# Kernel optimization log

Hardware: AMD Instinct MI355X
Metric: run time of the kernel (lower is better)

Reference implementation:

```python
import jax, jax.numpy as jnp
import numpy as np

D_MODEL = 1024
NUM_HEADS = 16
D_K = D_MODEL // NUM_HEADS
D_FF = 4096
EPS = 1e-5


def setup_inputs() -> dict:
    key = jax.random.key(0)
    ks = jax.random.split(key, 16)
    B, S = 2, 2048
    s_attn = 1.0 / np.sqrt(D_MODEL)
    s_ff1 = 1.0 / np.sqrt(D_MODEL)
    s_ff2 = 1.0 / np.sqrt(D_FF)
    return {
        "x": jax.random.normal(ks[0], (B, S, D_MODEL), jnp.float32),
        "Wq": jax.random.normal(ks[1], (D_MODEL, D_MODEL), jnp.float32) * s_attn,
        "bq": jnp.zeros((D_MODEL,), jnp.float32),
        "Wk": jax.random.normal(ks[2], (D_MODEL, D_MODEL), jnp.float32) * s_attn,
        "bk": jnp.zeros((D_MODEL,), jnp.float32),
        "Wv": jax.random.normal(ks[3], (D_MODEL, D_MODEL), jnp.float32) * s_attn,
        "bv": jnp.zeros((D_MODEL,), jnp.float32),
        "Wo": jax.random.normal(ks[4], (D_MODEL, D_MODEL), jnp.float32) * s_attn,
        "bo": jnp.zeros((D_MODEL,), jnp.float32),
        "W1": jax.random.normal(ks[5], (D_MODEL, D_FF), jnp.float32) * s_ff1,
        "b1": jnp.zeros((D_FF,), jnp.float32),
        "W2": jax.random.normal(ks[6], (D_FF, D_MODEL), jnp.float32) * s_ff2,
        "b2": jnp.zeros((D_MODEL,), jnp.float32),
        "g1": jnp.ones((D_MODEL,), jnp.float32),
        "be1": jnp.zeros((D_MODEL,), jnp.float32),
        "g2": jnp.ones((D_MODEL,), jnp.float32),
        "be2": jnp.zeros((D_MODEL,), jnp.float32),
    }


def _layernorm(x, g, b):
    m = jnp.mean(x, axis=-1, keepdims=True)
    v = jnp.mean(jnp.square(x - m), axis=-1, keepdims=True)
    return (x - m) * jax.lax.rsqrt(v + EPS) * g + b


def _split_heads(x, B, S):
    # (B, S, D) -> (B, H, S, d_k)
    return x.reshape(B, S, NUM_HEADS, D_K).transpose(0, 2, 1, 3)


def reference(x, Wq, bq, Wk, bk, Wv, bv, Wo, bo, W1, b1, W2, b2, g1, be1, g2, be2):
    B, S, _ = x.shape
    Q = _split_heads(x @ Wq + bq, B, S)
    K = _split_heads(x @ Wk + bk, B, S)
    V = _split_heads(x @ Wv + bv, B, S)
    scores = jnp.einsum("bhqd,bhkd->bhqk", Q, K) / np.sqrt(D_K).astype(np.float32)
    attn = jax.nn.softmax(scores, axis=-1)  # dropout is identity (p=0 / eval)
    ctx = jnp.einsum("bhqk,bhkd->bhqd", attn, V)
    ctx = ctx.transpose(0, 2, 1, 3).reshape(B, S, D_MODEL)
    attn_out = ctx @ Wo + bo
    h = _layernorm(x + attn_out, g1, be1)
    ff = jax.nn.relu(h @ W1 + b1) @ W2 + b2
    out = _layernorm(h + ff, g2, be2)
    return out, attn
```

## Files before the change

### kernel.cpp

```cpp
#include <hip/hip_runtime.h>
#include <cstddef>
#include <cstdint>

#define D_MODEL 1024
#define NUM_HEADS 16
#define DK 64
#define D_FF 4096
#define SEQ 2048
#define BATCH 2
#define EPS 1e-5f

typedef unsigned short u16;
typedef __attribute__((ext_vector_type(8))) short bf16x8;
typedef __attribute__((ext_vector_type(8))) unsigned short us8;
typedef __attribute__((ext_vector_type(4))) unsigned short us4;
typedef __attribute__((ext_vector_type(4))) float f32x4;

#define SBAR() asm volatile("s_barrier" ::: "memory")

__device__ __forceinline__ u16 f2b(float f) {
    unsigned u = __float_as_uint(f);
    u += 0x7fffu + ((u >> 16) & 1u);
    return (u16)(u >> 16);
}
__device__ __forceinline__ float b2f(u16 v) {
    return __uint_as_float((unsigned)v << 16);
}

__device__ __forceinline__ void gload16(const void* g, void* l) {
    __builtin_amdgcn_global_load_lds(
        (const __attribute__((address_space(1))) void*)g,
        (__attribute__((address_space(3))) void*)l, 16, 0, 0);
}

__device__ __forceinline__ void stage_half(
    const u16* __restrict__ g, int ld, long kbase, int h,
    u16* dst, int tid, int wid)
{
#pragma unroll
    for (int r = 0; r < 2; ++r) {
        const int ci  = r * 512 + tid;
        const int row = ci >> 2;
        const int wd  = ci & 3;
        const int f   = (row + (row >> 2)) & 3;
        const long src = (long)row * ld + kbase + (long)(h * 4 + (wd ^ f)) * 8;
        gload16(g + src, dst + (r * 512 + wid * 64) * 8);
    }
}

__device__ __forceinline__ bf16x8 frag64(const u16* base, int ks, int row, int g) {
    const int f = (row + (row >> 2)) & 3;
    return *(const bf16x8*)&base[ks * 8192 + row * 32 + ((g ^ f) * 8)];
}

template<int KTOT, bool RELU, int NSPLIT>
__global__ __launch_bounds__(512, 2) void gemm256(
    const u16* __restrict__ Abf, const u16* __restrict__ BT,
    const float* __restrict__ bias0, const float* __restrict__ bias1,
    const float* __restrict__ bias2,
    u16* __restrict__ C0, u16* __restrict__ C1, u16* __restrict__ C2,
    int ldc, int nx)
{
    constexpr int NT = KTOT / 64;
    __shared__ u16 lds[2][32768];

    const int tid = threadIdx.x;
    const int wid = tid >> 6, l = tid & 63;
    const int r16 = l & 15, g = l >> 4;
    const int wr = wid >> 2, wc = wid & 3;

    const int nwg = gridDim.x;
    const int q = nwg >> 3, rr = nwg & 7;
    const int xcd = blockIdx.x & 7, idx = blockIdx.x >> 3;
    const int wg = (xcd < rr ? xcd * (q + 1) : rr * (q + 1) + (xcd - rr) * q) + idx;
    const long bm = (long)(wg / nx) * 256;
    const long bn = (long)(wg % nx) * 256;

    const u16* Ag = Abf + bm * KTOT;
    const u16* Bg = BT + bn * KTOT;

    f32x4 acc[8][4];
#pragma unroll
    for (int i = 0; i < 8; ++i)
#pragma unroll
        for (int n = 0; n < 4; ++n)
            acc[i][n] = (f32x4){0.f, 0.f, 0.f, 0.f};

    stage_half(Ag, KTOT, 0, 0, &lds[0][0],     tid, wid);
    stage_half(Ag, KTOT, 0, 1, &lds[0][8192],  tid, wid);
    stage_half(Bg, KTOT, 0, 0, &lds[0][16384], tid, wid);
    stage_half(Bg, KTOT, 0, 1, &lds[0][24576], tid, wid);
    if (NT > 1) {
        stage_half(Ag, KTOT, 64, 0, &lds[1][0],     tid, wid);
        stage_half(Bg, KTOT, 64, 0, &lds[1][16384], tid, wid);
    }
    asm volatile("s_waitcnt vmcnt(4)" ::: "memory");
    SBAR();

    for (int t = 0; t < NT; ++t) {
        u16* cur = &lds[t & 1][0];
        u16* nxt = &lds[(t + 1) & 1][0];
        const long k1 = (long)(t + 1) * 64;
        const long k2 = (long)(t + 2) * 64;
        const bool s1 = (t + 1 < NT), s2 = (t + 2 < NT);

        bf16x8 a0[4], b0[4];
#pragma unroll
        for (int i = 0; i < 4; ++i) {
            a0[i] = frag64(cur,         0, wr * 128 + i * 16 + r16, g);
            b0[i] = frag64(cur + 16384, 0, wc * 64  + i * 16 + r16, g);
        }
        if (s1) stage_half(Ag, KTOT, k1, 1, nxt + 8192, tid, wid);
        SBAR();
        __builtin_amdgcn_s_setprio(1);
#pragma unroll
        for (int i = 0; i < 4; ++i)
#pragma unroll
            for (int n = 0; n < 4; ++n)
                acc[i][n] = __builtin_amdgcn_mfma_f32_16x16x32_bf16(
                    a0[i], b0[n], acc[i][n], 0, 0, 0);
        __builtin_amdgcn_s_setprio(0);
        SBAR();

        bf16x8 a1[4];
#pragma unroll
        for (int i = 0; i < 4; ++i)
            a1[i] = frag64(cur, 0, wr * 128 + (i + 4) * 16 + r16, g);
        if (s1) stage_half(Bg, KTOT, k1, 1, nxt + 24576, tid, wid);
        SBAR();
        __builtin_amdgcn_s_setprio(1);
#pragma unroll
        for (int i = 0; i < 4; ++i)
#pragma unroll
            for (int n = 0; n < 4; ++n)
                acc[i + 4][n] = __builtin_amdgcn_mfma_f32_16x16x32_bf16(
                    a1[i], b0[n], acc[i + 4][n], 0, 0, 0);
        __builtin_amdgcn_s_setprio(0);
        SBAR();

        bf16x8 a2[4], b1[4];
#pragma unroll
        for (int i = 0; i < 4; ++i) {
            a2[i] = frag64(cur,         1, wr * 128 + i * 16 + r16, g);
            b1[i] = frag64(cur + 16384, 1, wc * 64  + i * 16 + r16, g);
        }
        if (s2) stage_half(Ag, KTOT, k2, 0, cur, tid, wid);
        SBAR();
        __builtin_amdgcn_s_setprio(1);
#pragma unroll
        for (int i = 0; i < 4; ++i)
#pragma unroll
            for (int n = 0; n < 4; ++n)
                acc[i][n] = __builtin_amdgcn_mfma_f32_16x16x32_bf16(
                    a2[i], b1[n], acc[i][n], 0, 0, 0);
        __builtin_amdgcn_s_setprio(0);
        SBAR();

        bf16x8 a3[4];
#pragma unroll
        for (int i = 0; i < 4; ++i)
            a3[i] = frag64(cur, 1, wr * 128 + (i + 4) * 16 + r16, g);
        if (s2) stage_half(Bg, KTOT, k2, 0, cur + 16384, tid, wid);
        SBAR();
        __builtin_amdgcn_s_setprio(1);
#pragma unroll
        for (int i = 0; i < 4; ++i)
#pragma unroll
            for (int n = 0; n < 4; ++n)
                acc[i + 4][n] = __builtin_amdgcn_mfma_f32_16x16x32_bf16(
                    a3[i], b1[n], acc[i + 4][n], 0, 0, 0);
        __builtin_amdgcn_s_setprio(0);
        if (s2)      asm volatile("s_waitcnt vmcnt(4)" ::: "memory");
        else if (s1) asm volatile("s_waitcnt vmcnt(0)" ::: "memory");
        SBAR();
    }

    u16* Cb = C0; const float* bp = bias0; long coff = 0;
    if (NSPLIT == 3) {
        const int grp = (int)(bn >> 10);
        if (grp == 1)      { Cb = C1; bp = bias1; }
        else if (grp == 2) { Cb = C2; bp = bias2; }
        coff = (long)grp << 10;
    }
    const long crow0 = bm + wr * 128 + g * 4;
    const long ccol0 = bn + wc * 64 + r16 - coff;
#pragma unroll
    for (int n = 0; n < 4; ++n) {
        const long col = ccol0 + n * 16;
        const float bv = bp[col];
#pragma unroll
        for (int i = 0; i < 8; ++i)
#pragma unroll
            for (int j = 0; j < 4; ++j) {
                const long row = crow0 + i * 16 + j;
                float v = acc[i][n][j] + bv;
                if (RELU) v = fmaxf(v, 0.f);
                Cb[row * (long)ldc + col] = f2b(v);
            }
    }
}

template<int BM, int BN, int OM, bool RELU>
__global__ __launch_bounds__(256) void gemm_mfma(
    const u16* __restrict__ Abf, const u16* __restrict__ BT,
    const float* __restrict__ bias, void* __restrict__ Cout,
    int lda, int ldb, int ldc, int K, int nx)
{
    constexpr int WN = (BN >= 128) ? 2 : 1;
    constexpr int WM = 4 / WN;
    constexpr int MI = BM / (WM * 16);
    constexpr int NI = BN / (WN * 16);
    constexpr int RA = (BM * 4) / 256;
    constexpr int RB = (BN * 4) / 256;
    constexpr int TILE = (BM + BN) * 32;

    __shared__ u16 sm[2][TILE];

    const int tid = threadIdx.x;
    const int w = tid >> 6, l = tid & 63;
    const int r16 = l & 15, g = l >> 4;
    const int wr = w / WN, wc = w % WN;

    const int nwg = gridDim.x;
    const int q = nwg >> 3, rr = nwg & 7;
    const int xcd = blockIdx.x & 7, idx = blockIdx.x >> 3;
    const int wg = (xcd < rr ? xcd * (q + 1) : rr * (q + 1) + (xcd - rr) * q) + idx;
    const long bm = (long)(wg / nx) * BM;
    const long bn = (long)(wg % nx) * BN;

    f32x4 acc[MI][NI];
#pragma unroll
    for (int mi = 0; mi < MI; ++mi)
#pragma unroll
        for (int ni = 0; ni < NI; ++ni)
            acc[mi][ni] = (f32x4){0.f, 0.f, 0.f, 0.f};

    long aOff[RA], bOff[RB];
#pragma unroll
    for (int r = 0; r < RA; ++r) {
        int c = r * 256 + tid;
        aOff[r] = (long)(bm + (c >> 2)) * lda + (c & 3) * 8;
    }
#pragma unroll
    for (int r = 0; r < RB; ++r) {
        int c = r * 256 + tid;
        bOff[r] = (long)(bn + (c >> 2)) * ldb + (c & 3) * 8;
    }

#pragma unroll
    for (int r = 0; r < RA; ++r)
        gload16(Abf + aOff[r], &sm[0][0] + (r * 256 + w * 64) * 8);
#pragma unroll
    for (int r = 0; r < RB; ++r)
        gload16(BT + bOff[r], &sm[0][BM * 32] + (r * 256 + w * 64) * 8);
    __syncthreads();

    int cur = 0;
    for (int k0 = 0; k0 < K; k0 += 32) {
        if (k0 + 32 < K) {
            const int nxt = cur ^ 1;
#pragma unroll
            for (int r = 0; r < RA; ++r)
                gload16(Abf + aOff[r] + k0 + 32, &sm[nxt][0] + (r * 256 + w * 64) * 8);
#pragma unroll
            for (int r = 0; r < RB; ++r)
                gload16(BT + bOff[r] + k0 + 32, &sm[nxt][BM * 32] + (r * 256 + w * 64) * 8);
        }

        const u16* smA = &sm[cur][0];
        const u16* smB = &sm[cur][BM * 32];
        bf16x8 af[MI], bfr[NI];
#pragma unroll
        for (int mi = 0; mi < MI; ++mi)
            af[mi] = *(const bf16x8*)&smA[(wr * (MI * 16) + mi * 16 + r16) * 32 + g * 8];
#pragma unroll
        for (int ni = 0; ni < NI; ++ni)
            bfr[ni] = *(const bf16x8*)&smB[(wc * (NI * 16) + ni * 16 + r16) * 32 + g * 8];
#pragma unroll
        for (int mi = 0; mi < MI; ++mi)
#pragma unroll
            for (int ni = 0; ni < NI; ++ni)
                acc[mi][ni] = __builtin_amdgcn_mfma_f32_16x16x32_bf16(
                    af[mi], bfr[ni], acc[mi][ni], 0, 0, 0);

        __syncthreads();
        cur ^= 1;
    }

    float* Cf = (float*)Cout;
    u16*   Cb = (u16*)Cout;
    const long crow0 = bm + wr * (MI * 16) + g * 4;
    const long ccol0 = bn + wc * (NI * 16) + r16;
#pragma unroll
    for (int ni = 0; ni < NI; ++ni) {
        const long col = ccol0 + ni * 16;
        const float bv = bias ? bias[col] : 0.f;
#pragma unroll
        for (int mi = 0; mi < MI; ++mi) {
#pragma unroll
            for (int j = 0; j < 4; ++j) {
                const long row = crow0 + mi * 16 + j;
                float v = acc[mi][ni][j] + bv;
                if (RELU) v = fmaxf(v, 0.f);
                if (OM == 0) Cf[row * (long)ldc + col] = v;
                else         Cb[row * (long)ldc + col] = f2b(v);
            }
        }
    }
}

#define QBLK 128
#define KBLK 64
#define NTT (SEQ / KBLK)
#define C2E 0.18033688f

__global__ __launch_bounds__(256) void flash_attn(
    const u16* __restrict__ Qg, const u16* __restrict__ Kg,
    const u16* __restrict__ Vt, float* __restrict__ attn,
    u16* __restrict__ ctx)
{
    __shared__ u16 smem[16384];
    __shared__ u16 Ps[4][2048];
    __shared__ float stats[4][32];

    u16* const Qs  = smem;
    u16* const kb0 = smem + 8192;
    u16* const kb1 = smem;

    const int tid = threadIdx.x;
    const int w = tid >> 6, l = tid & 63;
    const int r16 = l & 15, g = l >> 4;

    const int wg = (blockIdx.x & 7) * (gridDim.x >> 3) + (blockIdx.x >> 3);
    const int qb = wg & 15, z = wg >> 4;
    const int b = z >> 4, h = z & 15;
    const long q0 = (long)qb * QBLK;

    const long kBase = ((long)b * SEQ) * D_MODEL + h * DK;
    const long vBase = (long)z * DK * SEQ;

#pragma unroll
    for (int r = 0; r < 4; ++r) {
        int c = r * 256 + tid;
        int row = c >> 3, bl = c & 7;
        long src = ((long)b * SEQ + q0 + row) * D_MODEL + h * DK
                 + ((bl ^ (row & 7)) * 8);
        gload16(Qg + src, Qs + (r * 256 + w * 64) * 8);
    }
#pragma unroll
    for (int r = 0; r < 2; ++r) {
        int c = r * 256 + tid;
        int row = c >> 3, bl = c & 7;
        gload16(Kg + kBase + (long)row * D_MODEL + ((bl ^ (row & 7)) * 8),
                kb0 + (r * 256 + w * 64) * 8);
    }
    __syncthreads();

    bf16x8 qf[2][2];
#pragma unroll
    for (int qi = 0; qi < 2; ++qi)
#pragma unroll
        for (int ks = 0; ks < 2; ++ks)
            qf[qi][ks] = *(const bf16x8*)
                &Qs[(w * 32 + qi * 16 + r16) * 64 + (((ks * 4 + g) ^ (r16 & 7)) * 8)];
    __syncthreads();

    float lrun[2] = {0.f, 0.f};

    for (int t = 0; t < NTT; ++t) {
        if (t + 1 < NTT) {
            u16* kdst = ((t + 1) & 1) ? kb1 : kb0;
            const long kro = (long)(t + 1) * KBLK;
#pragma unroll
            for (int r = 0; r < 2; ++r) {
                int c = r * 256 + tid;
                int row = c >> 3, bl = c & 7;
                gload16(Kg + kBase + (kro + row) * D_MODEL + ((bl ^ (row & 7)) * 8),
                        kdst + (r * 256 + w * 64) * 8);
            }
        }
        const u16* kcur = (t & 1) ? kb1 : kb0;

        f32x4 sT[4][2];
#pragma unroll
        for (int ki = 0; ki < 4; ++ki)
#pragma unroll
            for (int qi = 0; qi < 2; ++qi) sT[ki][qi] = (f32x4){0.f, 0.f, 0.f, 0.f};

        __builtin_amdgcn_s_setprio(1);
#pragma unroll
        for (int ks = 0; ks < 2; ++ks) {
            bf16x8 kf[4];
#pragma unroll
            for (int ki = 0; ki < 4; ++ki)
                kf[ki] = *(const bf16x8*)
                    &kcur[(ki * 16 + r16) * 64 + (((ks * 4 + g) ^ (r16 & 7)) * 8)];
#pragma unroll
            for (int ki = 0; ki < 4; ++ki)
#pragma unroll
                for (int qi = 0; qi < 2; ++qi)
                    sT[ki][qi] = __builtin_amdgcn_mfma_f32_16x16x32_bf16(
                        kf[ki], qf[qi][ks], sT[ki][qi], 0, 0, 0);
        }
        __builtin_amdgcn_s_setprio(0);

#pragma unroll
        for (int qi = 0; qi < 2; ++qi) {
            float ls = 0.f;
#pragma unroll
            for (int ki = 0; ki < 4; ++ki)
#pragma unroll
                for (int j = 0; j < 4; ++j)
                    ls += exp2f(sT[ki][qi][j] * C2E);
            ls += __shfl_xor(ls, 16);
            ls += __shfl_xor(ls, 32);
            lrun[qi] += ls;
        }
        __syncthreads();
    }

    u16* const p2b0 = smem + 8192;
    u16* const p2b1 = smem;
#pragma unroll
    for (int r = 0; r < 2; ++r) {
        int c = r * 256 + tid;
        int row = c >> 3, bl = c & 7;
        gload16(Kg + kBase + (long)row * D_MODEL + ((bl ^ (row & 7)) * 8),
                p2b0 + (r * 256 + w * 64) * 8);
        gload16(Vt + vBase + (long)row * SEQ + ((bl ^ (row & 7)) * 8),
                p2b0 + 4096 + (r * 256 + w * 64) * 8);
    }
    if (l < 16) {
        stats[w][r16]      = 1.0f / lrun[0];
        stats[w][16 + r16] = 1.0f / lrun[1];
    }
    __syncthreads();

    float il2[2][4];
#pragma unroll
    for (int mi = 0; mi < 2; ++mi)
#pragma unroll
        for (int j = 0; j < 4; ++j)
            il2[mi][j] = stats[w][mi * 16 + g * 4 + j];

    f32x4 acc2[2][4];
#pragma unroll
    for (int mi = 0; mi < 2; ++mi)
#pragma unroll
        for (int ni = 0; ni < 4; ++ni) acc2[mi][ni] = (f32x4){0.f, 0.f, 0.f, 0.f};

    for (int t = 0; t < NTT; ++t) {
        const int k0 = t * KBLK;
        if (t + 1 < NTT) {
            u16* dst = ((t + 1) & 1) ? p2b1 : p2b0;
            const long kro = (long)(t + 1) * KBLK;
#pragma unroll
            for (int r = 0; r < 2; ++r) {
                int c = r * 256 + tid;
                int row = c >> 3, bl = c & 7;
                gload16(Kg + kBase + (kro + row) * D_MODEL + ((bl ^ (row & 7)) * 8),
                        dst + (r * 256 + w * 64) * 8);
                gload16(Vt + vBase + (long)row * SEQ + kro + ((bl ^ (row & 7)) * 8),
                        dst + 4096 + (r * 256 + w * 64) * 8);
            }
        }
        const u16* kcur = (t & 1) ? p2b1 : p2b0;
        const u16* vcur = kcur + 4096;

        f32x4 s[2][4];
#pragma unroll
        for (int mi = 0; mi < 2; ++mi)
#pragma unroll
            for (int ni = 0; ni < 4; ++ni) s[mi][ni] = (f32x4){0.f, 0.f, 0.f, 0.f};

        __builtin_amdgcn_s_setprio(1);
#pragma unroll
        for (int ks = 0; ks < 2; ++ks) {
            bf16x8 kf[4];
#pragma unroll
            for (int ni = 0; ni < 4; ++ni)
                kf[ni] = *(const bf16x8*)
                    &kcur[(ni * 16 + r16) * 64 + (((ks * 4 + g) ^ (r16 & 7)) * 8)];
#pragma unroll
            for (int mi = 0; mi < 2; ++mi)
#pragma unroll
                for (int ni = 0; ni < 4; ++ni)
                    s[mi][ni] = __builtin_amdgcn_mfma_f32_16x16x32_bf16(
                        qf[mi][ks], kf[ni], s[mi][ni], 0, 0, 0);
        }
        __builtin_amdgcn_s_setprio(0);

#pragma unroll
        for (int mi = 0; mi < 2; ++mi)
#pragma unroll
            for (int j = 0; j < 4; ++j) {
                const int pr = mi * 16 + g * 4 + j;
                const long grow = (long)z * SEQ + q0 + w * 32 + pr;
#pragma unroll
                for (int ni = 0; ni < 4; ++ni) {
                    float p = exp2f(s[mi][ni][j] * C2E) * il2[mi][j];
                    const int pc = ni * 16 + r16;
                    attn[grow * SEQ + k0 + pc] = p;
                    Ps[w][pr * 64 + (pc ^ ((pr & 7) << 3))] = f2b(p);
                }
            }

        __builtin_amdgcn_s_setprio(1);
#pragma unroll
        for (int ks = 0; ks < 2; ++ks) {
            bf16x8 pf[2], vf[4];
#pragma unroll
            for (int mi = 0; mi < 2; ++mi)
                pf[mi] = *(const bf16x8*)
                    &Ps[w][(mi * 16 + r16) * 64 + (((ks * 4 + g) ^ (r16 & 7)) * 8)];
#pragma unroll
            for (int ni = 0; ni < 4; ++ni)
                vf[ni] = *(const bf16x8*)
                    &vcur[(ni * 16 + r16) * 64 + (((ks * 4 + g) ^ (r16 & 7)) * 8)];
#pragma unroll
            for (int mi = 0; mi < 2; ++mi)
#pragma unroll
                for (int ni = 0; ni < 4; ++ni)
                    acc2[mi][ni] = __builtin_amdgcn_mfma_f32_16x16x32_bf16(
                        pf[mi], vf[ni], acc2[mi][ni], 0, 0, 0);
        }
        __builtin_amdgcn_s_setprio(0);
        __syncthreads();
    }

#pragma unroll
    for (int mi = 0; mi < 2; ++mi)
#pragma unroll
        for (int j = 0; j < 4; ++j) {
            const long grow = (long)b * SEQ + q0 + w * 32 + mi * 16 + g * 4 + j;
#pragma unroll
            for (int ni = 0; ni < 4; ++ni)
                ctx[grow * D_MODEL + h * DK + ni * 16 + r16] = f2b(acc2[mi][ni][j]);
        }
}

__global__ __launch_bounds__(256) void cvt_bf16_kernel(
    const float* __restrict__ in, u16* __restrict__ out, long n)
{
    long i = ((long)blockIdx.x * 256 + threadIdx.x) * 8;
    if (i >= n) return;
    float4 a = *(const float4*)(in + i);
    float4 b = *(const float4*)(in + i + 4);
    us8 o;
    o[0] = f2b(a.x); o[1] = f2b(a.y); o[2] = f2b(a.z); o[3] = f2b(a.w);
    o[4] = f2b(b.x); o[5] = f2b(b.y); o[6] = f2b(b.z); o[7] = f2b(b.w);
    *(us8*)(out + i) = o;
}

__global__ __launch_bounds__(256) void transpose_cvt(
    const float* __restrict__ W, u16* __restrict__ Wt, int R, int C)
{
    __shared__ float t[32][33];
    const int tx = threadIdx.x & 31, ty = threadIdx.x >> 5;
    const long c = (long)blockIdx.x * 32 + tx;
    const long r0 = (long)blockIdx.y * 32;
#pragma unroll
    for (int j = 0; j < 32; j += 8)
        t[ty + j][tx] = W[(r0 + ty + j) * C + c];
    __syncthreads();
    const long r = r0 + tx;
#pragma unroll
    for (int j = 0; j < 32; j += 8)
        Wt[((long)blockIdx.x * 32 + ty + j) * R + r] = f2b(t[tx][ty + j]);
}

__global__ __launch_bounds__(256) void transpose_cvt4(
    const float* __restrict__ W0, const float* __restrict__ W1,
    const float* __restrict__ W2, const float* __restrict__ W3,
    u16* __restrict__ dst)
{
    __shared__ float t[32][33];
    const int z = blockIdx.z;
    const float* W = (z == 0) ? W0 : (z == 1) ? W1 : (z == 2) ? W2 : W3;
    u16* Wt = dst + (size_t)z * D_MODEL * D_MODEL;
    const int tx = threadIdx.x & 31, ty = threadIdx.x >> 5;
    const long c = (long)blockIdx.x * 32 + tx;
    const long r0 = (long)blockIdx.y * 32;
#pragma unroll
    for (int j = 0; j < 32; j += 8)
        t[ty + j][tx] = W[(r0 + ty + j) * D_MODEL + c];
    __syncthreads();
    const long r = r0 + tx;
#pragma unroll
    for (int j = 0; j < 32; j += 8)
        Wt[((long)blockIdx.x * 32 + ty + j) * D_MODEL + r] = f2b(t[tx][ty + j]);
}

__global__ __launch_bounds__(256) void transpose_v(
    const u16* __restrict__ V, u16* __restrict__ Vt)
{
    __shared__ u16 t[32][33];
    const int z = blockIdx.z, b = z >> 4, h = z & 15;
    const int tx = threadIdx.x & 31, ty = threadIdx.x >> 5;
    const long k0 = (long)blockIdx.x * 32;
    const long d0 = (long)blockIdx.y * 32;
#pragma unroll
    for (int j = 0; j < 32; j += 8)
        t[ty + j][tx] = V[((long)b * SEQ + k0 + ty + j) * D_MODEL + h * DK + d0 + tx];
    __syncthreads();
#pragma unroll
    for (int j = 0; j < 32; j += 8)
        Vt[((long)z * DK + d0 + ty + j) * SEQ + k0 + tx] = t[tx][ty + j];
}

template<bool BBF, bool WB>
__global__ __launch_bounds__(256) void add_ln_kernel(
    const float* __restrict__ a, const void* __restrict__ bsrc,
    const float* __restrict__ g, const float* __restrict__ be,
    float* __restrict__ out32, u16* __restrict__ outbf)
{
    const int l = threadIdx.x & 63, w = threadIdx.x >> 6;
    const long row = (long)blockIdx.x * 4 + w;
    const long base = row * D_MODEL;

    float xv[16];
#pragma unroll
    for (int c = 0; c < 4; ++c) {
        const long off = c * 256 + l * 4;
        float4 av = *(const float4*)(a + base + off);
        float4 bv;
        if (BBF) {
            us4 bb = *(const us4*)((const u16*)bsrc + base + off);
            bv.x = b2f(bb[0]); bv.y = b2f(bb[1]);
            bv.z = b2f(bb[2]); bv.w = b2f(bb[3]);
        } else {
            bv = *(const float4*)((const float*)bsrc + base + off);
        }
        xv[c * 4 + 0] = av.x + bv.x; xv[c * 4 + 1] = av.y + bv.y;
        xv[c * 4 + 2] = av.z + bv.z; xv[c * 4 + 3] = av.w + bv.w;
    }

    float s = 0.f;
#pragma unroll
    for (int i = 0; i < 16; ++i) s += xv[i];
#pragma unroll
    for (int off = 1; off < 64; off <<= 1) s += __shfl_xor(s, off);
    const float mean = s * (1.0f / D_MODEL);

    float ss = 0.f;
#pragma unroll
    for (int i = 0; i < 16; ++i) {
        xv[i] -= mean;
        ss += xv[i] * xv[i];
    }
#pragma unroll
    for (int off = 1; off < 64; off <<= 1) ss += __shfl_xor(ss, off);
    const float rs = rsqrtf(ss * (1.0f / D_MODEL) + EPS);

#pragma unroll
    for (int c = 0; c < 4; ++c) {
        const long off = c * 256 + l * 4;
        float4 gv = *(const float4*)(g + off);
        float4 bev = *(const float4*)(be + off);
        float4 o;
        o.x = xv[c * 4 + 0] * rs * gv.x + bev.x;
        o.y = xv[c * 4 + 1] * rs * gv.y + bev.y;
        o.z = xv[c * 4 + 2] * rs * gv.z + bev.z;
        o.w = xv[c * 4 + 3] * rs * gv.w + bev.w;
        *(float4*)&out32[base + off] = o;
        if (WB) {
            us4 ob;
            ob[0] = f2b(o.x); ob[1] = f2b(o.y);
            ob[2] = f2b(o.z); ob[3] = f2b(o.w);
            *(us4*)&outbf[base + off] = ob;
        }
    }
}

extern "C" void kernel_launch(void* const* d_in, const int* in_sizes, int n_in,
                              void* d_out, int out_size, void* d_ws, size_t ws_size,
                              hipStream_t stream)
{
    const float* x   = (const float*)d_in[0];
    const float* Wq  = (const float*)d_in[1];
    const float* bq  = (const float*)d_in[2];
    const float* Wk  = (const float*)d_in[3];
    const float* bk  = (const float*)d_in[4];
    const float* Wv  = (const float*)d_in[5];
    const float* bv  = (const float*)d_in[6];
    const float* Wo  = (const float*)d_in[7];
    const float* bo  = (const float*)d_in[8];
    const float* W1  = (const float*)d_in[9];
    const float* b1  = (const float*)d_in[10];
    const float* W2  = (const float*)d_in[11];
    const float* b2  = (const float*)d_in[12];
    const float* g1  = (const float*)d_in[13];
    const float* be1 = (const float*)d_in[14];
    const float* g2  = (const float*)d_in[15];
    const float* be2 = (const float*)d_in[16];

    float* out  = (float*)d_out;
    float* attn = out + (size_t)BATCH * SEQ * D_MODEL;

    char* ws = (char*)d_ws;
    const size_t MB = 1u << 20;
    u16* x_bf   = (u16*)(ws);
    u16* Q_bf   = (u16*)(ws + 8 * MB);
    u16* K_bf   = (u16*)(ws + 16 * MB);
    u16* V_bf   = (u16*)(ws + 24 * MB);
    u16* Vt     = (u16*)(ws + 32 * MB);
    u16* Wqt    = (u16*)(ws + 40 * MB);
    u16* Wot    = (u16*)(ws + 46 * MB);
    u16* W1t    = (u16*)(ws + 48 * MB);
    u16* W2t    = (u16*)(ws + 56 * MB);
    u16* ff1_bf = (u16*)(ws + 64 * MB);
    float* h32  = (float*)(ws + 112 * MB);
    u16* ctx_bf = x_bf;
    u16* h_bf   = K_bf;
    u16* ao_bf  = V_bf;
    u16* ff2_bf = Vt;

    const int M = BATCH * SEQ;
    const long MD = (long)M * D_MODEL;
    dim3 T(256);

    cvt_bf16_kernel<<<dim3(MD / 2048), T, 0, stream>>>(x, x_bf, MD);
    transpose_cvt4<<<dim3(32, 32, 4), T, 0, stream>>>(Wq, Wk, Wv, Wo, Wqt);
    transpose_cvt<<<dim3(D_FF / 32, D_MODEL / 32), T, 0, stream>>>(W1, W1t, D_MODEL, D_FF);
    transpose_cvt<<<dim3(D_MODEL / 32, D_FF / 32), T, 0, stream>>>(W2, W2t, D_FF, D_MODEL);

    gemm256<D_MODEL, false, 3><<<dim3((M / 256) * (3 * D_MODEL / 256)), dim3(512), 0, stream>>>(
        x_bf, Wqt, bq, bk, bv, Q_bf, K_bf, V_bf, D_MODEL, 3 * D_MODEL / 256);

    transpose_v<<<dim3(SEQ/32, DK/32, BATCH*NUM_HEADS), T, 0, stream>>>(V_bf, Vt);

    flash_attn<<<dim3((SEQ/QBLK) * BATCH * NUM_HEADS), T, 0, stream>>>(
        Q_bf, K_bf, Vt, attn, ctx_bf);

    gemm_mfma<128,128,1,false><<<dim3((D_MODEL/128) * (M/128)), T, 0, stream>>>(
        ctx_bf, Wot, bo, ao_bf, D_MODEL, D_MODEL, D_MODEL, D_MODEL, D_MODEL/128);

    add_ln_kernel<true,true><<<dim3(M/4), T, 0, stream>>>(x, ao_bf, g1, be1, h32, h_bf);

    gemm256<D_MODEL, true, 1><<<dim3((M / 256) * (D_FF / 256)), dim3(512), 0, stream>>>(
        h_bf, W1t, b1, nullptr, nullptr, ff1_bf, nullptr, nullptr, D_FF, D_FF / 256);

    gemm_mfma<128,128,1,false><<<dim3((D_MODEL/128) * (M/128)), T, 0, stream>>>(
        ff1_bf, W2t, b2, ff2_bf, D_FF, D_FF, D_MODEL, D_FF, D_MODEL/128);

    add_ln_kernel<true,false><<<dim3(M/4), T, 0, stream>>>(h32, ff2_bf, g2, be2, out, nullptr);
}
```

Measured before the change: 440.1 us.

## Merge preprocessing kernels, move QKV to 128-tile GEMM, use bf16 residuals in layernorm

Folds the x conversion and all four weight transposes into one preproc launch. The QKV projection moves from the 256x256 gemm256 kernel to the 128x128 gemm_mfma kernel with a three-way output split, which gives more workgroups. Both add+layernorm kernels now read bf16 residual inputs (x_bf, h_bf) instead of fp32 copies, removing the fp32 h buffer and its traffic at some cost in precision. The attention-probability output is written with nontemporal stores to limit cache pollution from the large attn tensor.

```diff
diff --git a/kernel.cpp b/kernel.cpp
--- a/kernel.cpp
+++ b/kernel.cpp
@@ -53,12 +53,10 @@
     return *(const bf16x8*)&base[ks * 8192 + row * 32 + ((g ^ f) * 8)];
 }
 
-template<int KTOT, bool RELU, int NSPLIT>
+template<int KTOT, bool RELU>
 __global__ __launch_bounds__(512, 2) void gemm256(
     const u16* __restrict__ Abf, const u16* __restrict__ BT,
-    const float* __restrict__ bias0, const float* __restrict__ bias1,
-    const float* __restrict__ bias2,
-    u16* __restrict__ C0, u16* __restrict__ C1, u16* __restrict__ C2,
+    const float* __restrict__ bias0, u16* __restrict__ C0,
     int ldc, int nx)
 {
     constexpr int NT = KTOT / 64;
@@ -175,6 +173,110 @@
         SBAR();
     }
 
+    const long crow0 = bm + wr * 128 + g * 4;
+    const long ccol0 = bn + wc * 64 + r16;
+#pragma unroll
+    for (int n = 0; n < 4; ++n) {
+        const long col = ccol0 + n * 16;
+        const float bv = bias0[col];
+#pragma unroll
+        for (int i = 0; i < 8; ++i)
+#pragma unroll
+            for (int j = 0; j < 4; ++j) {
+                const long row = crow0 + i * 16 + j;
+                float v = acc[i][n][j] + bv;
+                if (RELU) v = fmaxf(v, 0.f);
+                C0[row * (long)ldc + col] = f2b(v);
+            }
+    }
+}
+
+template<bool RELU, int NSPLIT>
+__global__ __launch_bounds__(256) void gemm_mfma(
+    const u16* __restrict__ Abf, const u16* __restrict__ BT,
+    const float* __restrict__ bias0, const float* __restrict__ bias1,
+    const float* __restrict__ bias2,
+    u16* __restrict__ C0, u16* __restrict__ C1, u16* __restrict__ C2,
+    int lda, int ldb, int ldc, int K, int nx)
+{
+    constexpr int BM = 128, BN = 128;
+    constexpr int MI = 4, NI = 4;
+    constexpr int RA = 2, RB = 2;
+    constexpr int TILE = (BM + BN) * 32;
+
+    __shared__ u16 sm[2][TILE];
+
+    const int tid = threadIdx.x;
+    const int w = tid >> 6, l = tid & 63;
+    const int r16 = l & 15, g = l >> 4;
+    const int wr = w >> 1, wc = w & 1;
+
+    const int nwg = gridDim.x;
+    const int q = nwg >> 3, rr = nwg & 7;
+    const int xcd = blockIdx.x & 7, idx = blockIdx.x >> 3;
+    const int wg = (xcd < rr ? xcd * (q + 1) : rr * (q + 1) + (xcd - rr) * q) + idx;
+    const long bm = (long)(wg / nx) * BM;
+    const long bn = (long)(wg % nx) * BN;
+
+    f32x4 acc[MI][NI];
+#pragma unroll
+    for (int mi = 0; mi < MI; ++mi)
+#pragma unroll
+        for (int ni = 0; ni < NI; ++ni)
+            acc[mi][ni] = (f32x4){0.f, 0.f, 0.f, 0.f};
+
+    long aOff[RA], bOff[RB];
+#pragma unroll
+    for (int r = 0; r < RA; ++r) {
+        int c = r * 256 + tid;
+        aOff[r] = (long)(bm + (c >> 2)) * lda + (c & 3) * 8;
+    }
+#pragma unroll
+    for (int r = 0; r < RB; ++r) {
+        int c = r * 256 + tid;
+        bOff[r] = (long)(bn + (c >> 2)) * ldb + (c & 3) * 8;
+    }
+
+#pragma unroll
+    for (int r = 0; r < RA; ++r)
+        gload16(Abf + aOff[r], &sm[0][0] + (r * 256 + w * 64) * 8);
+#pragma unroll
+    for (int r = 0; r < RB; ++r)
+        gload16(BT + bOff[r], &sm[0][BM * 32] + (r * 256 + w * 64) * 8);
+    __syncthreads();
+
+    int cur = 0;
+    for (int k0 = 0; k0 < K; k0 += 32) {
+        if (k0 + 32 < K) {
+            const int nxt = cur ^ 1;
+#pragma unroll
+            for (int r = 0; r < RA; ++r)
+                gload16(Abf + aOff[r] + k0 + 32, &sm[nxt][0] + (r * 256 + w * 64) * 8);
+#pragma unroll
+            for (int r = 0; r < RB; ++r)
+                gload16(BT + bOff[r] + k0 + 32, &sm[nxt][BM * 32] + (r * 256 + w * 64) * 8);
+        }
+
+        const u16* smA = &sm[cur][0];
+        const u16* smB = &sm[cur][BM * 32];
+        bf16x8 af[MI], bfr[NI];
+#pragma unroll
+        for (int mi = 0; mi < MI; ++mi)
+            af[mi] = *(const bf16x8*)&smA[(wr * 64 + mi * 16 + r16) * 32 + g * 8];
+#pragma unroll
+        for (int ni = 0; ni < NI; ++ni)
+            bfr[ni] = *(const bf16x8*)&smB[(wc * 64 + ni * 16 + r16) * 32 + g * 8];
+#pragma unroll
+        for (int mi = 0; mi < MI; ++mi)
+#pragma unroll
+            for (int ni = 0; ni < NI; ++ni)
+                acc[mi][ni] = __builtin_amdgcn_mfma_f32_16x16x32_bf16(
+                    af[mi], bfr[ni], acc[mi][ni], 0, 0, 0);
+
+        __syncthreads();
+        cur ^= 1;
+    }
+
     u16* Cb = C0; const float* bp = bias0; long coff = 0;
     if (NSPLIT == 3) {
         const int grp = (int)(bn >> 10);
@@ -182,119 +284,12 @@
         else if (grp == 2) { Cb = C2; bp = bias2; }
         coff = (long)grp << 10;
     }
-    const long crow0 = bm + wr * 128 + g * 4;
+    const long crow0 = bm + wr * 64 + g * 4;
     const long ccol0 = bn + wc * 64 + r16 - coff;
-#pragma unroll
-    for (int n = 0; n < 4; ++n) {
-        const long col = ccol0 + n * 16;
-        const float bv = bp[col];
-#pragma unroll
-        for (int i = 0; i < 8; ++i)
-#pragma unroll
-            for (int j = 0; j < 4; ++j) {
-                const long row = crow0 + i * 16 + j;
-                float v = acc[i][n][j] + bv;
-                if (RELU) v = fmaxf(v, 0.f);
-                Cb[row * (long)ldc + col] = f2b(v);
-            }
-    }
-}
-
-template<int BM, int BN, int OM, bool RELU>
-__global__ __launch_bounds__(256) void gemm_mfma(
-    const u16* __restrict__ Abf, const u16* __restrict__ BT,
-    const float* __restrict__ bias, void* __restrict__ Cout,
-    int lda, int ldb, int ldc, int K, int nx)
-{
-    constexpr int WN = (BN >= 128) ? 2 : 1;
-    constexpr int WM = 4 / WN;
-    constexpr int MI = BM / (WM * 16);
-    constexpr int NI = BN / (WN * 16);
-    constexpr int RA = (BM * 4) / 256;
-    constexpr int RB = (BN * 4) / 256;
-    constexpr int TILE = (BM + BN) * 32;
-
-    __shared__ u16 sm[2][TILE];
-
-    const int tid = threadIdx.x;
-    const int w = tid >> 6, l = tid & 63;
-    const int r16 = l & 15, g = l >> 4;
-    const int wr = w / WN, wc = w % WN;
-
-    const int nwg = gridDim.x;
-    const int q = nwg >> 3, rr = nwg & 7;
-    const int xcd = blockIdx.x & 7, idx = blockIdx.x >> 3;
-    const int wg = (xcd < rr ? xcd * (q + 1) : rr * (q + 1) + (xcd - rr) * q) + idx;
-    const long bm = (long)(wg / nx) * BM;
-    const long bn = (long)(wg % nx) * BN;
-
-    f32x4 acc[MI][NI];
-#pragma unroll
-    for (int mi = 0; mi < MI; ++mi)
-#pragma unroll
-        for (int ni = 0; ni < NI; ++ni)
-            acc[mi][ni] = (f32x4){0.f, 0.f, 0.f, 0.f};
-
-    long aOff[RA], bOff[RB];
-#pragma unroll
-    for (int r = 0; r < RA; ++r) {
-        int c = r * 256 + tid;
-        aOff[r] = (long)(bm + (c >> 2)) * lda + (c & 3) * 8;
-    }
-#pragma unroll
-    for (int r = 0; r < RB; ++r) {
-        int c = r * 256 + tid;
-        bOff[r] = (long)(bn + (c >> 2)) * ldb + (c & 3) * 8;
-    }
-
-#pragma unroll
-    for (int r = 0; r < RA; ++r)
-        gload16(Abf + aOff[r], &sm[0][0] + (r * 256 + w * 64) * 8);
-#pragma unroll
-    for (int r = 0; r < RB; ++r)
-        gload16(BT + bOff[r], &sm[0][BM * 32] + (r * 256 + w * 64) * 8);
-    __syncthreads();
-
-    int cur = 0;
-    for (int k0 = 0; k0 < K; k0 += 32) {
-        if (k0 + 32 < K) {
-            const int nxt = cur ^ 1;
-#pragma unroll
-            for (int r = 0; r < RA; ++r)
-                gload16(Abf + aOff[r] + k0 + 32, &sm[nxt][0] + (r * 256 + w * 64) * 8);
-#pragma unroll
-            for (int r = 0; r < RB; ++r)
-                gload16(BT + bOff[r] + k0 + 32, &sm[nxt][BM * 32] + (r * 256 + w * 64) * 8);
-        }
-
-        const u16* smA = &sm[cur][0];
-        const u16* smB = &sm[cur][BM * 32];
-        bf16x8 af[MI], bfr[NI];
-#pragma unroll
-        for (int mi = 0; mi < MI; ++mi)
-            af[mi] = *(const bf16x8*)&smA[(wr * (MI * 16) + mi * 16 + r16) * 32 + g * 8];
-#pragma unroll
-        for (int ni = 0; ni < NI; ++ni)
-            bfr[ni] = *(const bf16x8*)&smB[(wc * (NI * 16) + ni * 16 + r16) * 32 + g * 8];
-#pragma unroll
-        for (int mi = 0; mi < MI; ++mi)
-#pragma unroll
-            for (int ni = 0; ni < NI; ++ni)
-                acc[mi][ni] = __builtin_amdgcn_mfma_f32_16x16x32_bf16(
-                    af[mi], bfr[ni], acc[mi][ni], 0, 0, 0);
-
-        __syncthreads();
-        cur ^= 1;
-    }
-
-    float* Cf = (float*)Cout;
-    u16*   Cb = (u16*)Cout;
-    const long crow0 = bm + wr * (MI * 16) + g * 4;
-    const long ccol0 = bn + wc * (NI * 16) + r16;
 #pragma unroll
     for (int ni = 0; ni < NI; ++ni) {
         const long col = ccol0 + ni * 16;
-        const float bv = bias ? bias[col] : 0.f;
+        const float bv = bp[col];
 #pragma unroll
         for (int mi = 0; mi < MI; ++mi) {
 #pragma unroll
@@ -302,8 +297,7 @@
                 const long row = crow0 + mi * 16 + j;
                 float v = acc[mi][ni][j] + bv;
                 if (RELU) v = fmaxf(v, 0.f);
-                if (OM == 0) Cf[row * (long)ldc + col] = v;
-                else         Cb[row * (long)ldc + col] = f2b(v);
+                Cb[row * (long)ldc + col] = f2b(v);
             }
         }
     }
@@ -500,7 +494,7 @@
                 for (int ni = 0; ni < 4; ++ni) {
                     float p = exp2f(s[mi][ni][j] * C2E) * il2[mi][j];
                     const int pc = ni * 16 + r16;
-                    attn[grow * SEQ + k0 + pc] = p;
+                    __builtin_nontemporal_store(p, &attn[grow * SEQ + k0 + pc]);
                     Ps[w][pr * 64 + (pc ^ ((pr & 7) << 3))] = f2b(p);
                 }
             }
@@ -539,26 +533,12 @@
         }
 }
 
-__global__ __launch_bounds__(256) void cvt_bf16_kernel(
-    const float* __restrict__ in, u16* __restrict__ out, long n)
-{
-    long i = ((long)blockIdx.x * 256 + threadIdx.x) * 8;
-    if (i >= n) return;
-    float4 a = *(const float4*)(in + i);
-    float4 b = *(const float4*)(in + i + 4);
-    us8 o;
-    o[0] = f2b(a.x); o[1] = f2b(a.y); o[2] = f2b(a.z); o[3] = f2b(a.w);
-    o[4] = f2b(b.x); o[5] = f2b(b.y); o[6] = f2b(b.z); o[7] = f2b(b.w);
-    *(us8*)(out + i) = o;
-}
-
-__global__ __launch_bounds__(256) void transpose_cvt(
-    const float* __restrict__ W, u16* __restrict__ Wt, int R, int C)
-{
-    __shared__ float t[32][33];
-    const int tx = threadIdx.x & 31, ty = threadIdx.x >> 5;
-    const long c = (long)blockIdx.x * 32 + tx;
-    const long r0 = (long)blockIdx.y * 32;
+__device__ __forceinline__ void tr32(
+    const float* __restrict__ W, u16* __restrict__ Wt, int R, int C,
+    int bx, int by, int tx, int ty, float (*t)[33])
+{
+    const long c = (long)bx * 32 + tx;
+    const long r0 = (long)by * 32;
 #pragma unroll
     for (int j = 0; j < 32; j += 8)
         t[ty + j][tx] = W[(r0 + ty + j) * C + c];
@@ -566,29 +546,48 @@
     const long r = r0 + tx;
 #pragma unroll
     for (int j = 0; j < 32; j += 8)
-        Wt[((long)blockIdx.x * 32 + ty + j) * R + r] = f2b(t[tx][ty + j]);
-}
-
-__global__ __launch_bounds__(256) void transpose_cvt4(
-    const float* __restrict__ W0, const float* __restrict__ W1,
-    const float* __restrict__ W2, const float* __restrict__ W3,
-    u16* __restrict__ dst)
+        Wt[((long)bx * 32 + ty + j) * R + r] = f2b(t[tx][ty + j]);
+}
+
+__global__ __launch_bounds__(256) void preproc(
+    const float* __restrict__ x, u16* __restrict__ x_bf,
+    const float* __restrict__ Wq, const float* __restrict__ Wk,
+    const float* __restrict__ Wv, const float* __restrict__ Wo,
+    u16* __restrict__ Wqkvo_t,
+    const float* __restrict__ W1, u16* __restrict__ W1t,
+    const float* __restrict__ W2, u16* __restrict__ W2t)
 {
     __shared__ float t[32][33];
-    const int z = blockIdx.z;
-    const float* W = (z == 0) ? W0 : (z == 1) ? W1 : (z == 2) ? W2 : W3;
-    u16* Wt = dst + (size_t)z * D_MODEL * D_MODEL;
+    int bid = blockIdx.x;
     const int tx = threadIdx.x & 31, ty = threadIdx.x >> 5;
-    const long c = (long)blockIdx.x * 32 + tx;
-    const long r0 = (long)blockIdx.y * 32;
-#pragma unroll
-    for (int j = 0; j < 32; j += 8)
-        t[ty + j][tx] = W[(r0 + ty + j) * D_MODEL + c];
-    __syncthreads();
-    const long r = r0 + tx;
-#pragma unroll
-    for (int j = 0; j < 32; j += 8)
-        Wt[((long)blockIdx.x * 32 + ty + j) * D_MODEL + r] = f2b(t[tx][ty + j]);
+
+    if (bid < 2048) {
+        long i = ((long)bid * 256 + threadIdx.x) * 8;
+        float4 a = *(const float4*)(x + i);
+        float4 b = *(const float4*)(x + i + 4);
+        us8 o;
+        o[0] = f2b(a.x); o[1] = f2b(a.y); o[2] = f2b(a.z); o[3] = f2b(a.w);
+        o[4] = f2b(b.x); o[5] = f2b(b.y); o[6] = f2b(b.z); o[7] = f2b(b.w);
+        *(us8*)(x_bf + i) = o;
+        return;
+    }
+    bid -= 2048;
+    if (bid < 4096) {
+        const int z = bid >> 10, rem = bid & 1023;
+        const float* W = (z == 0) ? Wq : (z == 1) ? Wk : (z == 2) ? Wv : Wo;
+        tr32(W, Wqkvo_t + (size_t)z * D_MODEL * D_MODEL, D_MODEL, D_MODEL,
+             rem & 31, rem >> 5, tx, ty, t);
+        return;
+    }
+    bid -= 4096;
+    if (bid < 4096) {
+        tr32(W1, W1t, D_MODEL, D_FF, bid & 127, bid >> 7, tx, ty, t);
+        return;
+    }
+    bid -= 4096;
+    {
+        tr32(W2, W2t, D_FF, D_MODEL, bid & 31, bid >> 5, tx, ty, t);
+    }
 }
 
 __global__ __launch_bounds__(256) void transpose_v(
@@ -608,11 +607,11 @@
         Vt[((long)z * DK + d0 + ty + j) * SEQ + k0 + tx] = t[tx][ty + j];
 }
 
-template<bool BBF, bool WB>
+template<int OM>
 __global__ __launch_bounds__(256) void add_ln_kernel(
-    const float* __restrict__ a, const void* __restrict__ bsrc,
+    const u16* __restrict__ a, const u16* __restrict__ b,
     const float* __restrict__ g, const float* __restrict__ be,
-    float* __restrict__ out32, u16* __restrict__ outbf)
+    void* __restrict__ outp)
 {
     const int l = threadIdx.x & 63, w = threadIdx.x >> 6;
     const long row = (long)blockIdx.x * 4 + w;
@@ -620,19 +619,13 @@
 
     float xv[16];
 #pragma unroll
-    for (int c = 0; c < 4; ++c) {
-        const long off = c * 256 + l * 4;
-        float4 av = *(const float4*)(a + base + off);
-        float4 bv;
-        if (BBF) {
-            us4 bb = *(const us4*)((const u16*)bsrc + base + off);
-            bv.x = b2f(bb[0]); bv.y = b2f(bb[1]);
-            bv.z = b2f(bb[2]); bv.w = b2f(bb[3]);
-        } else {
-            bv = *(const float4*)((const float*)bsrc + base + off);
-        }
-        xv[c * 4 + 0] = av.x + bv.x; xv[c * 4 + 1] = av.y + bv.y;
-        xv[c * 4 + 2] = av.z + bv.z; xv[c * 4 + 3] = av.w + bv.w;
+    for (int c = 0; c < 2; ++c) {
+        const long off = c * 512 + l * 8;
+        us8 av = *(const us8*)(a + base + off);
+        us8 bv = *(const us8*)(b + base + off);
+#pragma unroll
+        for (int i = 0; i < 8; ++i)
+            xv[c * 8 + i] = b2f(av[i]) + b2f(bv[i]);
     }
 
     float s = 0.f;
@@ -653,21 +646,31 @@
     const float rs = rsqrtf(ss * (1.0f / D_MODEL) + EPS);
 
 #pragma unroll
-    for (int c = 0; c < 4; ++c) {
-        const long off = c * 256 + l * 4;
-        float4 gv = *(const float4*)(g + off);
-        float4 bev = *(const float4*)(be + off);
-        float4 o;
-        o.x = xv[c * 4 + 0] * rs * gv.x + bev.x;
-        o.y = xv[c * 4 + 1] * rs * gv.y + bev.y;
-        o.z = xv[c * 4 + 2] * rs * gv.z + bev.z;
-        o.w = xv[c * 4 + 3] * rs * gv.w + bev.w;
-        *(float4*)&out32[base + off] = o;
-        if (WB) {
-            us4 ob;
-            ob[0] = f2b(o.x); ob[1] = f2b(o.y);
-            ob[2] = f2b(o.z); ob[3] = f2b(o.w);
-            *(us4*)&outbf[base + off] = ob;
+    for (int c = 0; c < 2; ++c) {
+        const long off = c * 512 + l * 8;
+        float4 g0 = *(const float4*)(g + off);
+        float4 g1 = *(const float4*)(g + off + 4);
+        float4 b0 = *(const float4*)(be + off);
+        float4 b1 = *(const float4*)(be + off + 4);
+        float o[8];
+        o[0] = xv[c*8+0] * rs * g0.x + b0.x;
+        o[1] = xv[c*8+1] * rs * g0.y + b0.y;
+        o[2] = xv[c*8+2] * rs * g0.z + b0.z;
+        o[3] = xv[c*8+3] * rs * g0.w + b0.w;
+        o[4] = xv[c*8+4] * rs * g1.x + b1.x;
+        o[5] = xv[c*8+5] * rs * g1.y + b1.y;
+        o[6] = xv[c*8+6] * rs * g1.z + b1.z;
+        o[7] = xv[c*8+7] * rs * g1.w + b1.w;
+        if (OM == 0) {
+            float4 v0 = {o[0], o[1], o[2], o[3]};
+            float4 v1 = {o[4], o[5], o[6], o[7]};
+            *(float4*)((float*)outp + base + off) = v0;
+            *(float4*)((float*)outp + base + off + 4) = v1;
+        } else {
+            us8 ob;
+#pragma unroll
+            for (int i = 0; i < 8; ++i) ob[i] = f2b(o[i]);
+            *(us8*)((u16*)outp + base + off) = ob;
         }
     }
 }
@@ -699,49 +702,48 @@
 
     char* ws = (char*)d_ws;
     const size_t MB = 1u << 20;
-    u16* x_bf   = (u16*)(ws);
-    u16* Q_bf   = (u16*)(ws + 8 * MB);
-    u16* K_bf   = (u16*)(ws + 16 * MB);
-    u16* V_bf   = (u16*)(ws + 24 * MB);
-    u16* Vt     = (u16*)(ws + 32 * MB);
-    u16* Wqt    = (u16*)(ws + 40 * MB);
-    u16* Wot    = (u16*)(ws + 46 * MB);
-    u16* W1t    = (u16*)(ws + 48 * MB);
-    u16* W2t    = (u16*)(ws + 56 * MB);
-    u16* ff1_bf = (u16*)(ws + 64 * MB);
-    float* h32  = (float*)(ws + 112 * MB);
-    u16* ctx_bf = x_bf;
-    u16* h_bf   = K_bf;
-    u16* ao_bf  = V_bf;
-    u16* ff2_bf = Vt;
+    u16* x_bf    = (u16*)(ws);
+    u16* Q_bf    = (u16*)(ws + 8 * MB);
+    u16* K_bf    = (u16*)(ws + 16 * MB);
+    u16* V_bf    = (u16*)(ws + 24 * MB);
+    u16* Vt      = (u16*)(ws + 32 * MB);
+    u16* Wqkvo_t = (u16*)(ws + 40 * MB);
+    u16* W1t     = (u16*)(ws + 48 * MB);
+    u16* W2t     = (u16*)(ws + 56 * MB);
+    u16* ff1_bf  = (u16*)(ws + 64 * MB);
+    u16* ctx_bf  = (u16*)(ws + 96 * MB);
+    u16* Wot     = Wqkvo_t + (size_t)3 * D_MODEL * D_MODEL;
+    u16* h_bf    = K_bf;
+    u16* ao_bf   = V_bf;
+    u16* ff2_bf  = Vt;
 
     const int M = BATCH * SEQ;
-    const long MD = (long)M * D_MODEL;
     dim3 T(256);
 
-    cvt_bf16_kernel<<<dim3(MD / 2048), T, 0, stream>>>(x, x_bf, MD);
-    transpose_cvt4<<<dim3(32, 32, 4), T, 0, stream>>>(Wq, Wk, Wv, Wo, Wqt);
-    transpose_cvt<<<dim3(D_FF / 32, D_MODEL / 32), T, 0, stream>>>(W1, W1t, D_MODEL, D_FF);
-    transpose_cvt<<<dim3(D_MODEL / 32, D_FF / 32), T, 0, stream>>>(W2, W2t, D_FF, D_MODEL);
-
-    gemm256<D_MODEL, false, 3><<<dim3((M / 256) * (3 * D_MODEL / 256)), dim3(512), 0, stream>>>(
-        x_bf, Wqt, bq, bk, bv, Q_bf, K_bf, V_bf, D_MODEL, 3 * D_MODEL / 256);
-
-    transpose_v<<<dim3(SEQ/32, DK/32, BATCH*NUM_HEADS), T, 0, stream>>>(V_bf, Vt);
-
-    flash_attn<<<dim3((SEQ/QBLK) * BATCH * NUM_HEADS), T, 0, stream>>>(
+    preproc<<<dim3(2048 + 3 * 4096), T, 0, stream>>>(
+        x, x_bf, Wq, Wk, Wv, Wo, Wqkvo_t, W1, W1t, W2, W2t);
+
+    gemm_mfma<false, 3><<<dim3((M / 128) * 24), T, 0, stream>>>(
+        x_bf, Wqkvo_t, bq, bk, bv, Q_bf, K_bf, V_bf,
+        D_MODEL, D_MODEL, D_MODEL, D_MODEL, 24);
+
+    transpose_v<<<dim3(SEQ / 32, DK / 32, BATCH * NUM_HEADS), T, 0, stream>>>(V_bf, Vt);
+
+    flash_attn<<<dim3((SEQ / QBLK) * BATCH * NUM_HEADS), T, 0, stream>>>(
         Q_bf, K_bf, Vt, attn, ctx_bf);
 
-    gemm_mfma<128,128,1,false><<<dim3((D_MODEL/128) * (M/128)), T, 0, stream>>>(
-        ctx_bf, Wot, bo, ao_bf, D_MODEL, D_MODEL, D_MODEL, D_MODEL, D_MODEL/128);
-
-    add_ln_kernel<true,true><<<dim3(M/4), T, 0, stream>>>(x, ao_bf, g1, be1, h32, h_bf);
-
-    gemm256<D_MODEL, true, 1><<<dim3((M / 256) * (D_FF / 256)), dim3(512), 0, stream>>>(
-        h_bf, W1t, b1, nullptr, nullptr, ff1_bf, nullptr, nullptr, D_FF, D_FF / 256);
-
-    gemm_mfma<128,128,1,false><<<dim3((D_MODEL/128) * (M/128)), T, 0, stream>>>(
-        ff1_bf, W2t, b2, ff2_bf, D_FF, D_FF, D_MODEL, D_FF, D_MODEL/128);
-
-    add_ln_kernel<true,false><<<dim3(M/4), T, 0, stream>>>(h32, ff2_bf, g2, be2, out, nullptr);
-}
+    gemm_mfma<false, 1><<<dim3((M / 128) * 8), T, 0, stream>>>(
+        ctx_bf, Wot, bo, nullptr, nullptr, ao_bf, nullptr, nullptr,
+        D_MODEL, D_MODEL, D_MODEL, D_MODEL, 8);
+
+    add_ln_kernel<1><<<dim3(M / 4), T, 0, stream>>>(x_bf, ao_bf, g1, be1, h_bf);
+
+    gemm256<D_MODEL, true><<<dim3((M / 256) * (D_FF / 256)), dim3(512), 0, stream>>>(
+        h_bf, W1t, b1, ff1_bf, D_FF, D_FF / 256);
+
+    gemm_mfma<false, 1><<<dim3((M / 128) * 8), T, 0, stream>>>(
+        ff1_bf, W2t, b2, nullptr, nullptr, ff2_bf, nullptr, nullptr,
+        D_FF, D_FF, D_MODEL, D_FF, 8);
+
+    add_ln_kernel<0><<<dim3(M / 4), T, 0, stream>>>(h_bf, ff2_bf, g2, be2, out);
+}
```

Result: faster. 409.2 us (-7.0%).
